# Kernel tuning notes

Measured on AMD Instinct MI355X. Metric: run time of the kernel, lower is better.

Reference implementation:

```python
import jax, jax.numpy as jnp
import numpy as np

U = 256
B = 128
D = 256  # input_size


def _outer(a, b):
    # a,b: [B,U] -> [B,U,U]
    return a[:, :, None] * b[:, None, :]


def _hadamard_sigma(s1, s2, m1, m2):
    # sigma1*sigma2 + diag(m1) s2 diag(m1) + diag(m2) s1 diag(m2)
    return s1 * s2 + _outer(m1, m1) * s2 + _outer(m2, m2) * s1


def _w_t_Sigma_w(W, S):
    # W: [U,U], S: [B,U,U] -> W^T S W
    return jnp.einsum('ji,bjk,kl->bil', W, S, W)


def _x_Sigma_w_x_T(x, W_Sigma):
    # sum(x*x) scalar per batch times W_Sigma
    return jnp.sum(x * x, axis=1)[:, None, None] * W_Sigma


def _tr_Sigma(S, W_Sigma):
    return jnp.trace(S, axis1=1, axis2=2)[:, None, None] * W_Sigma


def setup_inputs() -> dict:
    key = jax.random.key(0)
    ks = jax.random.split(key, 16)
    inp = {
        'inputs': jax.random.normal(ks[0], (B, D), jnp.float32),
        'prev_state': jax.random.normal(ks[1], (B, U), jnp.float32),
        'Sigma_state': jax.random.normal(ks[2], (B, U, U), jnp.float32) * 0.05,
        'U_z': jax.random.normal(ks[3], (D, U), jnp.float32) * 0.05,
        'uz_sigma': jax.random.uniform(ks[4], (U,), jnp.float32, -12.0, -2.2),
        'W_z': jax.random.normal(ks[5], (U, U), jnp.float32) * 0.05,
        'wz_sigma': jax.random.uniform(ks[6], (U,), jnp.float32, -12.0, -2.2),
        'U_r': jax.random.normal(ks[7], (D, U), jnp.float32) * 0.05,
        'ur_sigma': jax.random.uniform(ks[8], (U,), jnp.float32, -12.0, -2.2),
        'W_r': jax.random.normal(ks[9], (U, U), jnp.float32) * 0.05,
        'wr_sigma': jax.random.uniform(ks[10], (U,), jnp.float32, -12.0, -2.2),
        'U_h': jax.random.normal(ks[11], (D, U), jnp.float32) * 0.05,
        'uh_sigma': jax.random.uniform(ks[12], (U,), jnp.float32, -12.0, -2.2),
        'W_h': jax.random.normal(ks[13], (U, U), jnp.float32) * 0.05,
        'wh_sigma': jax.random.uniform(ks[14], (U,), jnp.float32, -12.0, -2.2),
    }
    return inp


def reference(inputs, prev_state, Sigma_state, U_z, uz_sigma, W_z, wz_sigma,
              U_r, ur_sigma, W_r, wr_sigma, U_h, uh_sigma, W_h, wh_sigma):
    # z gate
    mz = inputs @ U_z + prev_state @ W_z
    z = jax.nn.sigmoid(mz)
    Uz_S = jnp.diag(jax.nn.softplus(uz_sigma))
    Wz_S = jnp.diag(jax.nn.softplus(wz_sigma))
    Sigma_zz = (_w_t_Sigma_w(W_z, Sigma_state)
                + _x_Sigma_w_x_T(prev_state, Wz_S)
                + _tr_Sigma(Sigma_state, Wz_S)
                + _x_Sigma_w_x_T(inputs, Uz_S))
    gz = z * (1.0 - z)  # d sigmoid
    Sigma_z = Sigma_zz * _outer(gz, gz)

    # r gate
    mr = inputs @ U_r + prev_state @ W_r
    r = jax.nn.sigmoid(mr)
    Ur_S = jnp.diag(jax.nn.softplus(ur_sigma))
    Wr_S = jnp.diag(jax.nn.softplus(wr_sigma))
    Sigma_rr = (_w_t_Sigma_w(W_r, Sigma_state)
                + _x_Sigma_w_x_T(prev_state, Wr_S)
                + _tr_Sigma(Sigma_state, Wr_S)
                + _x_Sigma_w_x_T(inputs, Ur_S))
    gr = r * (1.0 - r)
    Sigma_r = Sigma_rr * _outer(gr, gr)

    # candidate h
    sr = prev_state * r
    mh = inputs @ U_h + sr @ W_h
    h = jnp.tanh(mh)
    Uh_S = jnp.diag(jax.nn.softplus(uh_sigma))
    Wh_S = jnp.diag(jax.nn.softplus(wh_sigma))
    sigma_g = _hadamard_sigma(Sigma_state, Sigma_r, prev_state, r)
    Sigma_hh = (_w_t_Sigma_w(W_h, sigma_g)
                + _x_Sigma_w_x_T(sr, Wh_S)
                + _tr_Sigma(sigma_g, Wh_S)
                + _x_Sigma_w_x_T(inputs, Uh_S))
    gh = 1.0 - h * h  # d tanh
    Sigma_h = Sigma_hh * _outer(gh, gh)

    # output mean and covariance
    mu_out = z * prev_state + (1.0 - z) * h
    sigma_a = _hadamard_sigma(Sigma_z, Sigma_state, z, prev_state)
    sigma_b = _hadamard_sigma(Sigma_z, Sigma_h, 1.0 - z, h)
    sigma_ab = Sigma_z * _outer(prev_state, h)
    sigma_abT = Sigma_z * _outer(h, prev_state)
    Sigma_out = sigma_a + sigma_b - sigma_ab - sigma_abT
    return mu_out, Sigma_out
```

## Files before the change

kernel.cpp:

```cpp
#include <hip/hip_runtime.h>
#include <math.h>


typedef __attribute__((ext_vector_type(8))) short sh8;
typedef __attribute__((ext_vector_type(4))) float f4;
typedef __attribute__((ext_vector_type(4))) unsigned short us4;

__device__ __forceinline__ unsigned short f2bf(float f) {
  unsigned int u = __float_as_uint(f);
  u = (u + 0x7fffu + ((u >> 16) & 1u)) >> 16;
  return (unsigned short)u;
}
__device__ __forceinline__ float bf2f(unsigned short u) {
  return __uint_as_float(((unsigned int)u) << 16);
}
__device__ __forceinline__ f4 mfma16(sh8 a, sh8 b, f4 c) {
  return __builtin_amdgcn_mfma_f32_16x16x32_bf16(a, b, c, 0, 0, 0);
}


__global__ __launch_bounds__(256) void prep_kernel(
    const float* __restrict__ xin, const float* __restrict__ prev,
    const float* __restrict__ S,
    const float* __restrict__ Uz, const float* __restrict__ Wz,
    const float* __restrict__ uzs, const float* __restrict__ wzs,
    const float* __restrict__ Ur, const float* __restrict__ Wr,
    const float* __restrict__ urs, const float* __restrict__ wrs,
    const float* __restrict__ Uh, const float* __restrict__ Wh,
    const float* __restrict__ uhs, const float* __restrict__ whs,
    unsigned short* __restrict__ Sfrag, unsigned short* __restrict__ packs,
    float* __restrict__ spzw, float* __restrict__ spzu,
    float* __restrict__ sprw, float* __restrict__ spru,
    float* __restrict__ sphw, float* __restrict__ sphu,
    float* __restrict__ sxA, float* __restrict__ spA, float* __restrict__ trSA,
    float* __restrict__ zv, float* __restrict__ rv,
    float* __restrict__ gzv, float* __restrict__ grv)
{
  const int blk = blockIdx.x, t = threadIdx.x;
  __shared__ float Srows[16][260];
  __shared__ float xs[256], ps[256];

  if (blk < 2048) {
    const int b = blk >> 4, R = blk & 15;
    const float* Sb = S + ((size_t)b << 16) + (size_t)(R * 16) * 256;
#pragma unroll
    for (int i = 0; i < 4; ++i) {
      int e = t + i * 256;
      int row = e >> 6, c4 = e & 63;
      f4 v = reinterpret_cast<const f4*>(Sb)[e];
      *reinterpret_cast<f4*>(&Srows[row][c4 * 4]) = v;
    }
    __syncthreads();
    unsigned short* outb = Sfrag + ((size_t)b << 16) + R * 512;
#pragma unroll
    for (int qi = 0; qi < 2; ++qi) {
      int q = t + qi * 256;
      int kt = q >> 6, lane = q & 63;
      int l15 = lane & 15, c0 = kt * 32 + (lane >> 4) * 8;
      union { unsigned short u[8]; uint4 v; } pk;
#pragma unroll
      for (int e = 0; e < 8; ++e) pk.u[e] = f2bf(Srows[l15][c0 + e]);
      *reinterpret_cast<uint4*>(outb + kt * 8192 + lane * 8) = pk.v;
    }
    return;
  }

  if (blk < 2096) {
    int gid = (blk - 2048) * 256 + t;
#pragma unroll
    for (int q2 = 0; q2 < 4; ++q2) {
      int cid = gid * 4 + q2;
      int p = cid >> 13, c = cid & 8191;
      const float* W = (p >> 1) == 0 ? Wz : ((p >> 1) == 1 ? Wr : Wh);
      int lane = c & 63, l15 = lane & 15, lhi = lane >> 4;
      int n, k8;
      if ((p & 1) == 0) {
        int nb = (c >> 11) & 3, kt = (c >> 8) & 7, ct = (c >> 6) & 3;
        n = nb * 64 + ct * 16 + l15; k8 = kt * 32 + lhi * 8;
      } else {
        int wv = (c >> 11) & 3, rt = (c >> 9) & 3, jt = (c >> 6) & 7;
        n = wv * 64 + rt * 16 + l15; k8 = jt * 32 + lhi * 8;
      }
      union { unsigned short u[8]; uint4 v; } pk;
#pragma unroll
      for (int e = 0; e < 8; ++e) pk.u[e] = f2bf(W[(k8 + e) * 256 + n]);
      *reinterpret_cast<uint4*>(packs + (size_t)p * 65536 + (size_t)c * 8) = pk.v;
    }
    return;
  }

  if (blk < 2224) {
    const int b = blk - 2096;
    __shared__ float red[12];
    float x = xin[b * 256 + t];
    float p = prev[b * 256 + t];
    float d = S[(size_t)b * 65536 + (size_t)t * 257];
    float a0 = x * x, a1 = p * p, a2 = d;
#pragma unroll
    for (int off = 32; off; off >>= 1) {
      a0 += __shfl_down(a0, off, 64);
      a1 += __shfl_down(a1, off, 64);
      a2 += __shfl_down(a2, off, 64);
    }
    if ((t & 63) == 0) {
      int w = t >> 6;
      red[w] = a0; red[4 + w] = a1; red[8 + w] = a2;
    }
    __syncthreads();
    if (t == 0) {
      sxA[b] = red[0] + red[1] + red[2] + red[3];
      spA[b] = red[4] + red[5] + red[6] + red[7];
      trSA[b] = red[8] + red[9] + red[10] + red[11];
    }
    return;
  }

  if (blk == 2224) {
    spzw[t] = log1pf(expf(wzs[t])); spzu[t] = log1pf(expf(uzs[t]));
    sprw[t] = log1pf(expf(wrs[t])); spru[t] = log1pf(expf(urs[t]));
    sphw[t] = log1pf(expf(whs[t])); sphu[t] = log1pf(expf(uhs[t]));
    return;
  }

  const int q = blk - 2225, g = q >> 7, b = q & 127;
  xs[t] = xin[b * 256 + t];
  ps[t] = prev[b * 256 + t];
  __syncthreads();
  const float* U = g ? Ur : Uz;
  const float* W = g ? Wr : Wz;
  float a0 = 0.f, a1 = 0.f, a2 = 0.f, a3 = 0.f;
  for (int k = 0; k < 256; k += 4) {
    a0 = fmaf(xs[k],     U[(k)     * 256 + t], a0);
    a1 = fmaf(xs[k + 1], U[(k + 1) * 256 + t], a1);
    a2 = fmaf(xs[k + 2], U[(k + 2) * 256 + t], a2);
    a3 = fmaf(xs[k + 3], U[(k + 3) * 256 + t], a3);
  }
  for (int k = 0; k < 256; k += 4) {
    a0 = fmaf(ps[k],     W[(k)     * 256 + t], a0);
    a1 = fmaf(ps[k + 1], W[(k + 1) * 256 + t], a1);
    a2 = fmaf(ps[k + 2], W[(k + 2) * 256 + t], a2);
    a3 = fmaf(ps[k + 3], W[(k + 3) * 256 + t], a3);
  }
  const float m = (a0 + a1) + (a2 + a3);
  const float zz = 1.f / (1.f + expf(-m));
  const int idx = b * 256 + t;
  if (g == 0) { zv[idx] = zz; gzv[idx] = zz * (1.f - zz); }
  else        { rv[idx] = zz; grv[idx] = zz * (1.f - zz); }
}

__global__ __launch_bounds__(256, 2) void fuse_kernel(
    const float* __restrict__ xin, const float* __restrict__ prev,
    const float* __restrict__ S,
    const float* __restrict__ Uh, const float* __restrict__ Wh,
    const float* __restrict__ zv, const float* __restrict__ rv,
    const float* __restrict__ gzv, const float* __restrict__ grv,
    const unsigned short* __restrict__ packs,
    const unsigned short* __restrict__ Sfrag,
    const float* __restrict__ spzw, const float* __restrict__ spzu,
    const float* __restrict__ sprw, const float* __restrict__ spru,
    const float* __restrict__ sxA, const float* __restrict__ spA,
    const float* __restrict__ trSA,
    unsigned short* __restrict__ Szbf, unsigned short* __restrict__ sgf,
    float* __restrict__ trsgP,
    float* __restrict__ ghv, float* __restrict__ pmhv,
    float* __restrict__ muOut, float* __restrict__ ssrA)
{
  __shared__ unsigned short Ttz[64][264];
  __shared__ unsigned short Ttr[64][264];
  __shared__ float ev0z[256], evdz[256], ev0r[256], evdr[256];
  __shared__ float ev2[256], ev3[256];

  const int blk = blockIdx.x, tid = threadIdx.x;
  const f4 z4 = {0.f, 0.f, 0.f, 0.f};

  if (blk < 128) {
    float* xs  = (float*)&Ttz[0][0];
    float* ps  = xs + 256;
    float* srs = ps + 256;
    float* red = srs + 256;
    const int b = blk, t = tid;
    xs[t] = xin[b * 256 + t];
    float pv = prev[b * 256 + t];
    ps[t] = pv;
    srs[t] = pv * rv[b * 256 + t];
    __syncthreads();
    float a0 = 0.f, a1 = 0.f, a2 = 0.f, a3 = 0.f;
    for (int k = 0; k < 256; k += 4) {
      a0 = fmaf(xs[k],     Uh[(k)     * 256 + t], a0);
      a1 = fmaf(xs[k + 1], Uh[(k + 1) * 256 + t], a1);
      a2 = fmaf(xs[k + 2], Uh[(k + 2) * 256 + t], a2);
      a3 = fmaf(xs[k + 3], Uh[(k + 3) * 256 + t], a3);
    }
    for (int k = 0; k < 256; k += 4) {
      a0 = fmaf(srs[k],     Wh[(k)     * 256 + t], a0);
      a1 = fmaf(srs[k + 1], Wh[(k + 1) * 256 + t], a1);
      a2 = fmaf(srs[k + 2], Wh[(k + 2) * 256 + t], a2);
      a3 = fmaf(srs[k + 3], Wh[(k + 3) * 256 + t], a3);
    }
    const float m = (a0 + a1) + (a2 + a3);
    const float h = tanhf(m);
    const int idx = b * 256 + t;
    const float z = zv[idx];
    ghv[idx]  = 1.f - h * h;
    pmhv[idx] = pv - h;
    muOut[idx] = z * pv + (1.f - z) * h;
    float s = srs[t] * srs[t];
#pragma unroll
    for (int off = 32; off; off >>= 1) s += __shfl_down(s, off, 64);
    __syncthreads();
    if ((t & 63) == 0) red[t >> 6] = s;
    __syncthreads();
    if (t == 0) ssrA[b] = red[0] + red[1] + red[2] + red[3];
    return;
  }

  const int q = blk - 128;
  const int c = q & 7, nb = (q >> 3) & 3, chunk = q >> 5;
  const int b = chunk * 8 + c;
  const int col0 = nb * 64;
  const int wave = tid >> 6, lane = tid & 63, lhi = lane >> 4, l15 = lane & 15;
  const size_t bb = (size_t)b << 16;
  const unsigned short* p1z = packs;
  const unsigned short* p2z = packs + (size_t)1 * 65536;
  const unsigned short* p1r = packs + (size_t)2 * 65536;
  const unsigned short* p2r = packs + (size_t)3 * 65536;

  {
    const int u = tid;
    const float sd = spA[b] + trSA[b], sx = sxA[b];
    ev0z[u] = gzv[b * 256 + u];
    evdz[u] = sd * spzw[u] + sx * spzu[u];
    ev0r[u] = grv[b * 256 + u];
    evdr[u] = sd * sprw[u] + sx * spru[u];
    ev2[u]  = prev[b * 256 + u];
    ev3[u]  = rv[b * 256 + u];
  }

  f4 az[4][4], ar[4][4];
#pragma unroll
  for (int i = 0; i < 4; ++i)
#pragma unroll
    for (int j = 0; j < 4; ++j) { az[i][j] = z4; ar[i][j] = z4; }

  const unsigned short* Af = Sfrag + bb;
#pragma unroll
  for (int kt = 0; kt < 8; ++kt) {
    sh8 af[4], bz[4], br[4];
#pragma unroll
    for (int rt = 0; rt < 4; ++rt)
      af[rt] = *reinterpret_cast<const sh8*>(
          Af + kt * 8192 + (wave * 4 + rt) * 512 + lane * 8);
#pragma unroll
    for (int ct = 0; ct < 4; ++ct) {
      const size_t po = (size_t)(((nb * 8 + kt) * 4 + ct) * 64 + lane) << 3;
      bz[ct] = *reinterpret_cast<const sh8*>(p1z + po);
      br[ct] = *reinterpret_cast<const sh8*>(p1r + po);
    }
#pragma unroll
    for (int rt = 0; rt < 4; ++rt)
#pragma unroll
      for (int ct = 0; ct < 4; ++ct) {
        az[rt][ct] = mfma16(af[rt], bz[ct], az[rt][ct]);
        ar[rt][ct] = mfma16(af[rt], br[ct], ar[rt][ct]);
      }
  }

#pragma unroll
  for (int rt = 0; rt < 4; ++rt) {
    const int row0 = wave * 64 + rt * 16 + lhi * 4;
#pragma unroll
    for (int ct = 0; ct < 4; ++ct) {
      const int cc = ct * 16 + l15;
      us4 pz, pr;
      pz[0] = f2bf(az[rt][ct][0]); pz[1] = f2bf(az[rt][ct][1]);
      pz[2] = f2bf(az[rt][ct][2]); pz[3] = f2bf(az[rt][ct][3]);
      pr[0] = f2bf(ar[rt][ct][0]); pr[1] = f2bf(ar[rt][ct][1]);
      pr[2] = f2bf(ar[rt][ct][2]); pr[3] = f2bf(ar[rt][ct][3]);
      *reinterpret_cast<us4*>(&Ttz[cc][row0]) = pz;
      *reinterpret_cast<us4*>(&Ttr[cc][row0]) = pr;
    }
  }
  __syncthreads();

#pragma unroll
  for (int i = 0; i < 4; ++i)
#pragma unroll
    for (int j = 0; j < 4; ++j) { az[i][j] = z4; ar[i][j] = z4; }

#pragma unroll
  for (int jt = 0; jt < 8; ++jt) {
    const int j8 = jt * 32 + lhi * 8;
    sh8 a2z[4], a2r[4], bz[4], br[4];
#pragma unroll
    for (int rt = 0; rt < 4; ++rt) {
      const size_t po = (size_t)(((wave * 4 + rt) * 8 + jt) * 64 + lane) << 3;
      a2z[rt] = *reinterpret_cast<const sh8*>(p2z + po);
      a2r[rt] = *reinterpret_cast<const sh8*>(p2r + po);
    }
#pragma unroll
    for (int ct = 0; ct < 4; ++ct) {
      bz[ct] = *reinterpret_cast<const sh8*>(&Ttz[ct * 16 + l15][j8]);
      br[ct] = *reinterpret_cast<const sh8*>(&Ttr[ct * 16 + l15][j8]);
    }
#pragma unroll
    for (int rt = 0; rt < 4; ++rt)
#pragma unroll
      for (int ct = 0; ct < 4; ++ct) {
        az[rt][ct] = mfma16(a2z[rt], bz[ct], az[rt][ct]);
        ar[rt][ct] = mfma16(a2r[rt], br[ct], ar[rt][ct]);
      }
  }

  float trloc = 0.f;
#pragma unroll
  for (int rt = 0; rt < 4; ++rt) {
    const int i0 = wave * 64 + rt * 16 + lhi * 4;
#pragma unroll
    for (int ct = 0; ct < 4; ++ct) {
      const int j = col0 + ct * 16 + l15;
#pragma unroll
      for (int rr = 0; rr < 4; ++rr) {
        const int i = i0 + rr;
        const size_t idx = bb + ((size_t)i << 8) + j;
        float Yz = az[rt][ct][rr] + ((i == j) ? evdz[i] : 0.f);
        Szbf[idx] = f2bf(Yz * ev0z[i] * ev0z[j]);
        float Yr = ar[rt][ct][rr] + ((i == j) ? evdr[i] : 0.f);
        float Sr = Yr * ev0r[i] * ev0r[j];
        float Sv = S[idx];
        float sgv = Sr * (Sv + ev2[i] * ev2[j]) + ev3[i] * ev3[j] * Sv;
        size_t fo = bb + (size_t)((j >> 5) * 8192) + (size_t)((i >> 4) * 512)
                  + (size_t)((((j >> 3) & 3) * 16 + (i & 15)) * 8) + (j & 7);
        sgf[fo] = f2bf(sgv);
        if (i == j) trloc += sgv;
      }
    }
  }

  if (wave == nb) {
#pragma unroll
    for (int off = 32; off; off >>= 1) trloc += __shfl_down(trloc, off, 64);
    if (lane == 0) trsgP[b * 4 + nb] = trloc;
  }
}

__global__ __launch_bounds__(256) void gateh_kernel(
    const float* __restrict__ S,
    const unsigned short* __restrict__ sgf,
    const unsigned short* __restrict__ packs,
    const unsigned short* __restrict__ Szb,
    const float* __restrict__ ghv, const float* __restrict__ zv,
    const float* __restrict__ pmhv,
    const float* __restrict__ sphw, const float* __restrict__ sphu,
    const float* __restrict__ sxA, const float* __restrict__ ssrA,
    const float* __restrict__ trsgIn,
    float* __restrict__ fOut)
{
  __shared__ unsigned short Tt[64][264];
  __shared__ float ev0[256], evd[256], ev2[256], ev3[256];

  const int blk = blockIdx.x, tid = threadIdx.x;
  const int wave = tid >> 6, lane = tid & 63, lhi = lane >> 4, l15 = lane & 15;
  const int c = blk & 7, nb = (blk >> 3) & 3, chunk = blk >> 5;
  const int b = chunk * 8 + c, col0 = nb * 64;
  const size_t bb = (size_t)b << 16;
  const f4 z4 = {0.f, 0.f, 0.f, 0.f};
  const unsigned short* p1 = packs + (size_t)4 * 65536;
  const unsigned short* p2 = packs + (size_t)5 * 65536;

  {
    const int u = tid;
    float trsg = trsgIn[b * 4] + trsgIn[b * 4 + 1]
               + trsgIn[b * 4 + 2] + trsgIn[b * 4 + 3];
    ev0[u] = ghv[b * 256 + u];
    evd[u] = (ssrA[b] + trsg) * sphw[u] + sxA[b] * sphu[u];
    ev2[u] = zv[b * 256 + u];
    ev3[u] = pmhv[b * 256 + u];
  }

  f4 acc[4][4];
#pragma unroll
  for (int i = 0; i < 4; ++i)
#pragma unroll
    for (int j = 0; j < 4; ++j) acc[i][j] = z4;

  const unsigned short* Af = sgf + bb;
#pragma unroll
  for (int kt = 0; kt < 8; ++kt) {
    sh8 af[4], bfr[4];
#pragma unroll
    for (int rt = 0; rt < 4; ++rt)
      af[rt] = *reinterpret_cast<const sh8*>(
          Af + kt * 8192 + (wave * 4 + rt) * 512 + lane * 8);
#pragma unroll
    for (int ct = 0; ct < 4; ++ct)
      bfr[ct] = *reinterpret_cast<const sh8*>(
          p1 + ((size_t)(((nb * 8 + kt) * 4 + ct) * 64 + lane) << 3));
#pragma unroll
    for (int rt = 0; rt < 4; ++rt)
#pragma unroll
      for (int ct = 0; ct < 4; ++ct)
        acc[rt][ct] = mfma16(af[rt], bfr[ct], acc[rt][ct]);
  }

#pragma unroll
  for (int rt = 0; rt < 4; ++rt) {
    const int row0 = wave * 64 + rt * 16 + lhi * 4;
#pragma unroll
    for (int ct = 0; ct < 4; ++ct) {
      const int cc = ct * 16 + l15;
      us4 p4;
      p4[0] = f2bf(acc[rt][ct][0]); p4[1] = f2bf(acc[rt][ct][1]);
      p4[2] = f2bf(acc[rt][ct][2]); p4[3] = f2bf(acc[rt][ct][3]);
      *reinterpret_cast<us4*>(&Tt[cc][row0]) = p4;
    }
  }
  __syncthreads();

#pragma unroll
  for (int i = 0; i < 4; ++i)
#pragma unroll
    for (int j = 0; j < 4; ++j) acc[i][j] = z4;

#pragma unroll
  for (int jt = 0; jt < 8; ++jt) {
    const int j8 = jt * 32 + lhi * 8;
    sh8 af[4], bfr[4];
#pragma unroll
    for (int rt = 0; rt < 4; ++rt)
      af[rt] = *reinterpret_cast<const sh8*>(
          p2 + ((size_t)(((wave * 4 + rt) * 8 + jt) * 64 + lane) << 3));
#pragma unroll
    for (int ct = 0; ct < 4; ++ct)
      bfr[ct] = *reinterpret_cast<const sh8*>(&Tt[ct * 16 + l15][j8]);
#pragma unroll
    for (int rt = 0; rt < 4; ++rt)
#pragma unroll
      for (int ct = 0; ct < 4; ++ct)
        acc[rt][ct] = mfma16(af[rt], bfr[ct], acc[rt][ct]);
  }

#pragma unroll
  for (int rt = 0; rt < 4; ++rt) {
    const int i0 = wave * 64 + rt * 16 + lhi * 4;
#pragma unroll
    for (int ct = 0; ct < 4; ++ct) {
      const int j = col0 + ct * 16 + l15;
#pragma unroll
      for (int rr = 0; rr < 4; ++rr) {
        const int i = i0 + rr;
        const size_t idx = bb + ((size_t)i << 8) + j;
        float Sh = (acc[rt][ct][rr] + ((i == j) ? evd[i] : 0.f)) * ev0[i] * ev0[j];
        float Sv = S[idx];
        float Szv = bf2f(Szb[idx]);
        fOut[idx] = Szv * (Sv + Sh + ev3[i] * ev3[j])
                  + Sv * ev2[i] * ev2[j]
                  + Sh * (1.f - ev2[i]) * (1.f - ev2[j]);
      }
    }
  }
}

extern "C" void kernel_launch(void* const* d_in, const int* in_sizes, int n_in,
                              void* d_out, int out_size, void* d_ws, size_t ws_size,
                              hipStream_t stream)
{
  const float* xin  = (const float*)d_in[0];
  const float* prev = (const float*)d_in[1];
  const float* S    = (const float*)d_in[2];
  const float* Uz = (const float*)d_in[3];  const float* uzs = (const float*)d_in[4];
  const float* Wz = (const float*)d_in[5];  const float* wzs = (const float*)d_in[6];
  const float* Ur = (const float*)d_in[7];  const float* urs = (const float*)d_in[8];
  const float* Wr = (const float*)d_in[9];  const float* wrs = (const float*)d_in[10];
  const float* Uh = (const float*)d_in[11]; const float* uhs = (const float*)d_in[12];
  const float* Wh = (const float*)d_in[13]; const float* whs = (const float*)d_in[14];

  float* muOut  = (float*)d_out;
  float* SigOut = muOut + 128 * 256;

  char* p = (char*)d_ws;
  auto take = [&](size_t bytes) { void* q = (void*)p; p += bytes; return q; };
  unsigned short* Sfrag = (unsigned short*)take(16777216);
  unsigned short* sgf   = (unsigned short*)take(16777216);
  unsigned short* Szbf  = (unsigned short*)take(16777216);
  unsigned short* packs = (unsigned short*)take(786432);
  float* zv   = (float*)take(131072);
  float* rv   = (float*)take(131072);
  float* gzv  = (float*)take(131072);
  float* grv  = (float*)take(131072);
  float* ghv  = (float*)take(131072);
  float* pmhv = (float*)take(131072);
  float* spzw = (float*)take(1024);
  float* spzu = (float*)take(1024);
  float* sprw = (float*)take(1024);
  float* spru = (float*)take(1024);
  float* sphw = (float*)take(1024);
  float* sphu = (float*)take(1024);
  float* sxA  = (float*)take(512);
  float* spA  = (float*)take(512);
  float* trSA = (float*)take(512);
  float* ssrA = (float*)take(512);
  float* trsgP = (float*)take(2048);
  (void)in_sizes; (void)n_in; (void)out_size; (void)ws_size;

  prep_kernel<<<2481, 256, 0, stream>>>(
      xin, prev, S, Uz, Wz, uzs, wzs, Ur, Wr, urs, wrs, Uh, Wh, uhs, whs,
      Sfrag, packs, spzw, spzu, sprw, spru, sphw, sphu,
      sxA, spA, trSA, zv, rv, gzv, grv);

  fuse_kernel<<<640, 256, 0, stream>>>(
      xin, prev, S, Uh, Wh, zv, rv, gzv, grv, packs, Sfrag,
      spzw, spzu, sprw, spru, sxA, spA, trSA,
      Szbf, sgf, trsgP, ghv, pmhv, muOut, ssrA);

  gateh_kernel<<<512, 256, 0, stream>>>(
      S, sgf, packs, Szbf, ghv, zv, pmhv, sphw, sphu,
      sxA, ssrA, trsgP, SigOut);
}
```

Baseline: 90.69 us.

## Split fuse and gateh row tiles across eight waves per block

Result: slower. 94.63 us (+4.3%).

```diff
diff --git a/kernel.cpp b/kernel.cpp
--- a/kernel.cpp
+++ b/kernel.cpp
@@ -148,7 +148,7 @@
   else        { rv[idx] = zz; grv[idx] = zz * (1.f - zz); }
 }
 
-__global__ __launch_bounds__(256, 2) void fuse_kernel(
+__global__ __launch_bounds__(512, 4) void fuse_kernel(
     const float* __restrict__ xin, const float* __restrict__ prev,
     const float* __restrict__ S,
     const float* __restrict__ Uh, const float* __restrict__ Wh,
@@ -179,38 +179,46 @@
     float* srs = ps + 256;
     float* red = srs + 256;
     const int b = blk, t = tid;
-    xs[t] = xin[b * 256 + t];
-    float pv = prev[b * 256 + t];
-    ps[t] = pv;
-    srs[t] = pv * rv[b * 256 + t];
+    float pv = 0.f;
+    if (t < 256) {
+      xs[t] = xin[b * 256 + t];
+      pv = prev[b * 256 + t];
+      ps[t] = pv;
+      srs[t] = pv * rv[b * 256 + t];
+    }
     __syncthreads();
-    float a0 = 0.f, a1 = 0.f, a2 = 0.f, a3 = 0.f;
-    for (int k = 0; k < 256; k += 4) {
-      a0 = fmaf(xs[k],     Uh[(k)     * 256 + t], a0);
-      a1 = fmaf(xs[k + 1], Uh[(k + 1) * 256 + t], a1);
-      a2 = fmaf(xs[k + 2], Uh[(k + 2) * 256 + t], a2);
-      a3 = fmaf(xs[k + 3], Uh[(k + 3) * 256 + t], a3);
-    }
-    for (int k = 0; k < 256; k += 4) {
-      a0 = fmaf(srs[k],     Wh[(k)     * 256 + t], a0);
-      a1 = fmaf(srs[k + 1], Wh[(k + 1) * 256 + t], a1);
-      a2 = fmaf(srs[k + 2], Wh[(k + 2) * 256 + t], a2);
-      a3 = fmaf(srs[k + 3], Wh[(k + 3) * 256 + t], a3);
-    }
-    const float m = (a0 + a1) + (a2 + a3);
-    const float h = tanhf(m);
-    const int idx = b * 256 + t;
-    const float z = zv[idx];
-    ghv[idx]  = 1.f - h * h;
-    pmhv[idx] = pv - h;
-    muOut[idx] = z * pv + (1.f - z) * h;
-    float s = srs[t] * srs[t];
+    float s = 0.f;
+    if (t < 256) {
+      float a0 = 0.f, a1 = 0.f, a2 = 0.f, a3 = 0.f;
+      for (int k = 0; k < 256; k += 4) {
+        a0 = fmaf(xs[k],     Uh[(k)     * 256 + t], a0);
+        a1 = fmaf(xs[k + 1], Uh[(k + 1) * 256 + t], a1);
+        a2 = fmaf(xs[k + 2], Uh[(k + 2) * 256 + t], a2);
+        a3 = fmaf(xs[k + 3], Uh[(k + 3) * 256 + t], a3);
+      }
+      for (int k = 0; k < 256; k += 4) {
+        a0 = fmaf(srs[k],     Wh[(k)     * 256 + t], a0);
+        a1 = fmaf(srs[k + 1], Wh[(k + 1) * 256 + t], a1);
+        a2 = fmaf(srs[k + 2], Wh[(k + 2) * 256 + t], a2);
+        a3 = fmaf(srs[k + 3], Wh[(k + 3) * 256 + t], a3);
+      }
+      const float m = (a0 + a1) + (a2 + a3);
+      const float h = tanhf(m);
+      const int idx = b * 256 + t;
+      const float z = zv[idx];
+      ghv[idx]  = 1.f - h * h;
+      pmhv[idx] = pv - h;
+      muOut[idx] = z * pv + (1.f - z) * h;
+      s = srs[t] * srs[t];
+    }
 #pragma unroll
     for (int off = 32; off; off >>= 1) s += __shfl_down(s, off, 64);
     __syncthreads();
     if ((t & 63) == 0) red[t >> 6] = s;
     __syncthreads();
-    if (t == 0) ssrA[b] = red[0] + red[1] + red[2] + red[3];
+    if (t == 0)
+      ssrA[b] = ((red[0] + red[1]) + (red[2] + red[3]))
+              + ((red[4] + red[5]) + (red[6] + red[7]));
     return;
   }
 
@@ -218,14 +226,14 @@
   const int c = q & 7, nb = (q >> 3) & 3, chunk = q >> 5;
   const int b = chunk * 8 + c;
   const int col0 = nb * 64;
-  const int wave = tid >> 6, lane = tid & 63, lhi = lane >> 4, l15 = lane & 15;
+  const int w = tid >> 6, lane = tid & 63, lhi = lane >> 4, l15 = lane & 15;
   const size_t bb = (size_t)b << 16;
   const unsigned short* p1z = packs;
   const unsigned short* p2z = packs + (size_t)1 * 65536;
   const unsigned short* p1r = packs + (size_t)2 * 65536;
   const unsigned short* p2r = packs + (size_t)3 * 65536;
 
-  {
+  if (tid < 256) {
     const int u = tid;
     const float sd = spA[b] + trSA[b], sx = sxA[b];
     ev0z[u] = gzv[b * 256 + u];
@@ -236,20 +244,20 @@
     ev3[u]  = rv[b * 256 + u];
   }
 
-  f4 az[4][4], ar[4][4];
-#pragma unroll
-  for (int i = 0; i < 4; ++i)
+  f4 az[2][4], ar[2][4];
+#pragma unroll
+  for (int i = 0; i < 2; ++i)
 #pragma unroll
     for (int j = 0; j < 4; ++j) { az[i][j] = z4; ar[i][j] = z4; }
 
   const unsigned short* Af = Sfrag + bb;
 #pragma unroll
   for (int kt = 0; kt < 8; ++kt) {
-    sh8 af[4], bz[4], br[4];
-#pragma unroll
-    for (int rt = 0; rt < 4; ++rt)
+    sh8 af[2], bz[4], br[4];
+#pragma unroll
+    for (int rt = 0; rt < 2; ++rt)
       af[rt] = *reinterpret_cast<const sh8*>(
-          Af + kt * 8192 + (wave * 4 + rt) * 512 + lane * 8);
+          Af + kt * 8192 + (w * 2 + rt) * 512 + lane * 8);
 #pragma unroll
     for (int ct = 0; ct < 4; ++ct) {
       const size_t po = (size_t)(((nb * 8 + kt) * 4 + ct) * 64 + lane) << 3;
@@ -257,7 +265,7 @@
       br[ct] = *reinterpret_cast<const sh8*>(p1r + po);
     }
 #pragma unroll
-    for (int rt = 0; rt < 4; ++rt)
+    for (int rt = 0; rt < 2; ++rt)
 #pragma unroll
       for (int ct = 0; ct < 4; ++ct) {
         az[rt][ct] = mfma16(af[rt], bz[ct], az[rt][ct]);
@@ -266,8 +274,8 @@
   }
 
 #pragma unroll
-  for (int rt = 0; rt < 4; ++rt) {
-    const int row0 = wave * 64 + rt * 16 + lhi * 4;
+  for (int rt = 0; rt < 2; ++rt) {
+    const int row0 = w * 32 + rt * 16 + lhi * 4;
 #pragma unroll
     for (int ct = 0; ct < 4; ++ct) {
       const int cc = ct * 16 + l15;
@@ -283,17 +291,17 @@
   __syncthreads();
 
 #pragma unroll
-  for (int i = 0; i < 4; ++i)
+  for (int i = 0; i < 2; ++i)
 #pragma unroll
     for (int j = 0; j < 4; ++j) { az[i][j] = z4; ar[i][j] = z4; }
 
 #pragma unroll
   for (int jt = 0; jt < 8; ++jt) {
     const int j8 = jt * 32 + lhi * 8;
-    sh8 a2z[4], a2r[4], bz[4], br[4];
-#pragma unroll
-    for (int rt = 0; rt < 4; ++rt) {
-      const size_t po = (size_t)(((wave * 4 + rt) * 8 + jt) * 64 + lane) << 3;
+    sh8 a2z[2], a2r[2], bz[4], br[4];
+#pragma unroll
+    for (int rt = 0; rt < 2; ++rt) {
+      const size_t po = (size_t)(((w * 2 + rt) * 8 + jt) * 64 + lane) << 3;
       a2z[rt] = *reinterpret_cast<const sh8*>(p2z + po);
       a2r[rt] = *reinterpret_cast<const sh8*>(p2r + po);
     }
@@ -303,7 +311,7 @@
       br[ct] = *reinterpret_cast<const sh8*>(&Ttr[ct * 16 + l15][j8]);
     }
 #pragma unroll
-    for (int rt = 0; rt < 4; ++rt)
+    for (int rt = 0; rt < 2; ++rt)
 #pragma unroll
       for (int ct = 0; ct < 4; ++ct) {
         az[rt][ct] = mfma16(a2z[rt], bz[ct], az[rt][ct]);
@@ -313,8 +321,8 @@
 
   float trloc = 0.f;
 #pragma unroll
-  for (int rt = 0; rt < 4; ++rt) {
-    const int i0 = wave * 64 + rt * 16 + lhi * 4;
+  for (int rt = 0; rt < 2; ++rt) {
+    const int i0 = w * 32 + rt * 16 + lhi * 4;
 #pragma unroll
     for (int ct = 0; ct < 4; ++ct) {
       const int j = col0 + ct * 16 + l15;
@@ -336,14 +344,14 @@
     }
   }
 
-  if (wave == nb) {
+  if ((w >> 1) == nb) {
 #pragma unroll
     for (int off = 32; off; off >>= 1) trloc += __shfl_down(trloc, off, 64);
-    if (lane == 0) trsgP[b * 4 + nb] = trloc;
-  }
-}
-
-__global__ __launch_bounds__(256) void gateh_kernel(
+    if (lane == 0) trsgP[b * 8 + w] = trloc;
+  }
+}
+
+__global__ __launch_bounds__(512, 4) void gateh_kernel(
     const float* __restrict__ S,
     const unsigned short* __restrict__ sgf,
     const unsigned short* __restrict__ packs,
@@ -359,7 +367,7 @@
   __shared__ float ev0[256], evd[256], ev2[256], ev3[256];
 
   const int blk = blockIdx.x, tid = threadIdx.x;
-  const int wave = tid >> 6, lane = tid & 63, lhi = lane >> 4, l15 = lane & 15;
+  const int w = tid >> 6, lane = tid & 63, lhi = lane >> 4, l15 = lane & 15;
   const int c = blk & 7, nb = (blk >> 3) & 3, chunk = blk >> 5;
   const int b = chunk * 8 + c, col0 = nb * 64;
   const size_t bb = (size_t)b << 16;
@@ -367,44 +375,45 @@
   const unsigned short* p1 = packs + (size_t)4 * 65536;
   const unsigned short* p2 = packs + (size_t)5 * 65536;
 
-  {
+  if (tid < 256) {
     const int u = tid;
-    float trsg = trsgIn[b * 4] + trsgIn[b * 4 + 1]
-               + trsgIn[b * 4 + 2] + trsgIn[b * 4 + 3];
+    float trsg = 0.f;
+#pragma unroll
+    for (int qq = 0; qq < 8; ++qq) trsg += trsgIn[b * 8 + qq];
     ev0[u] = ghv[b * 256 + u];
     evd[u] = (ssrA[b] + trsg) * sphw[u] + sxA[b] * sphu[u];
     ev2[u] = zv[b * 256 + u];
     ev3[u] = pmhv[b * 256 + u];
   }
 
-  f4 acc[4][4];
-#pragma unroll
-  for (int i = 0; i < 4; ++i)
+  f4 acc[2][4];
+#pragma unroll
+  for (int i = 0; i < 2; ++i)
 #pragma unroll
     for (int j = 0; j < 4; ++j) acc[i][j] = z4;
 
   const unsigned short* Af = sgf + bb;
 #pragma unroll
   for (int kt = 0; kt < 8; ++kt) {
-    sh8 af[4], bfr[4];
-#pragma unroll
-    for (int rt = 0; rt < 4; ++rt)
+    sh8 af[2], bfr[4];
+#pragma unroll
+    for (int rt = 0; rt < 2; ++rt)
       af[rt] = *reinterpret_cast<const sh8*>(
-          Af + kt * 8192 + (wave * 4 + rt) * 512 + lane * 8);
+          Af + kt * 8192 + (w * 2 + rt) * 512 + lane * 8);
 #pragma unroll
     for (int ct = 0; ct < 4; ++ct)
       bfr[ct] = *reinterpret_cast<const sh8*>(
           p1 + ((size_t)(((nb * 8 + kt) * 4 + ct) * 64 + lane) << 3));
 #pragma unroll
-    for (int rt = 0; rt < 4; ++rt)
+    for (int rt = 0; rt < 2; ++rt)
 #pragma unroll
       for (int ct = 0; ct < 4; ++ct)
         acc[rt][ct] = mfma16(af[rt], bfr[ct], acc[rt][ct]);
   }
 
 #pragma unroll
-  for (int rt = 0; rt < 4; ++rt) {
-    const int row0 = wave * 64 + rt * 16 + lhi * 4;
+  for (int rt = 0; rt < 2; ++rt) {
+    const int row0 = w * 32 + rt * 16 + lhi * 4;
 #pragma unroll
     for (int ct = 0; ct < 4; ++ct) {
       const int cc = ct * 16 + l15;
@@ -417,31 +426,31 @@
   __syncthreads();
 
 #pragma unroll
-  for (int i = 0; i < 4; ++i)
+  for (int i = 0; i < 2; ++i)
 #pragma unroll
     for (int j = 0; j < 4; ++j) acc[i][j] = z4;
 
 #pragma unroll
   for (int jt = 0; jt < 8; ++jt) {
     const int j8 = jt * 32 + lhi * 8;
-    sh8 af[4], bfr[4];
-#pragma unroll
-    for (int rt = 0; rt < 4; ++rt)
+    sh8 af[2], bfr[4];
+#pragma unroll
+    for (int rt = 0; rt < 2; ++rt)
       af[rt] = *reinterpret_cast<const sh8*>(
-          p2 + ((size_t)(((wave * 4 + rt) * 8 + jt) * 64 + lane) << 3));
+          p2 + ((size_t)(((w * 2 + rt) * 8 + jt) * 64 + lane) << 3));
 #pragma unroll
     for (int ct = 0; ct < 4; ++ct)
       bfr[ct] = *reinterpret_cast<const sh8*>(&Tt[ct * 16 + l15][j8]);
 #pragma unroll
-    for (int rt = 0; rt < 4; ++rt)
+    for (int rt = 0; rt < 2; ++rt)
 #pragma unroll
       for (int ct = 0; ct < 4; ++ct)
         acc[rt][ct] = mfma16(af[rt], bfr[ct], acc[rt][ct]);
   }
 
 #pragma unroll
-  for (int rt = 0; rt < 4; ++rt) {
-    const int i0 = wave * 64 + rt * 16 + lhi * 4;
+  for (int rt = 0; rt < 2; ++rt) {
+    const int i0 = w * 32 + rt * 16 + lhi * 4;
 #pragma unroll
     for (int ct = 0; ct < 4; ++ct) {
       const int j = col0 + ct * 16 + l15;
@@ -499,7 +508,7 @@
   float* spA  = (float*)take(512);
   float* trSA = (float*)take(512);
   float* ssrA = (float*)take(512);
-  float* trsgP = (float*)take(2048);
+  float* trsgP = (float*)take(4096);
   (void)in_sizes; (void)n_in; (void)out_size; (void)ws_size;
 
   prep_kernel<<<2481, 256, 0, stream>>>(
@@ -507,12 +516,12 @@
       Sfrag, packs, spzw, spzu, sprw, spru, sphw, sphu,
       sxA, spA, trSA, zv, rv, gzv, grv);
 
-  fuse_kernel<<<640, 256, 0, stream>>>(
+  fuse_kernel<<<640, 512, 0, stream>>>(
       xin, prev, S, Uh, Wh, zv, rv, gzv, grv, packs, Sfrag,
       spzw, spzu, sprw, spru, sxA, spA, trSA,
       Szbf, sgf, trsgP, ghv, pmhv, muOut, ssrA);
 
-  gateh_kernel<<<512, 256, 0, stream>>>(
+  gateh_kernel<<<512, 512, 0, stream>>>(
       S, sgf, packs, Szbf, ghv, zv, pmhv, sphw, sphu,
       sxA, ssrA, trsgP, SigOut);
 }
```
